# Kernel optimization log

Hardware: AMD Instinct MI355X
Metric: run time of the kernel (lower is better)

Reference implementation:

```python
import jax, jax.numpy as jnp
import numpy as np

VOXEL_SIZE = 96
SHARPNESS = 100.0
EPS = 1e-8


def _grid_coords(V):
    # matches torch: x fastest, normalized by (V-1); shape [V*V, 2] as (x, y)
    y, x = jnp.meshgrid(jnp.arange(V, dtype=jnp.float32), jnp.arange(V, dtype=jnp.float32), indexing='ij')
    return jnp.stack([x.ravel(), y.ravel()], axis=1) / float(V - 1)


def setup_inputs() -> dict:
    key = jax.random.key(0)
    k1, k2, k3 = jax.random.split(key, 3)
    B, N, P = 4, 32, 32
    polygons = jax.random.uniform(k1, (B, N, P, 2), dtype=jnp.float32)
    attributes = jax.random.uniform(k2, (B, 8), dtype=jnp.float32)
    validity_scores = jax.random.uniform(k3, (B, N), dtype=jnp.float32)
    return {"polygons": polygons, "attributes": attributes, "validity_scores": validity_scores}


def _polygon_masks(polygons, coords):
    # polygons: [B,N,P,2], coords: [M,2] -> soft occupancy masks [B,N,M]
    v0 = polygons                              # [B,N,P,2]
    v1 = jnp.roll(polygons, -1, axis=2)        # next vertex (closed loop)
    e = v1 - v0                                # edges [B,N,P,2]
    pts = coords[None, None, None]             # [1,1,1,M,2]
    v = pts - v0[:, :, :, None, :]             # [B,N,P,M,2]
    e_sq = (e * e).sum(-1) + EPS               # [B,N,P]
    t = (v * e[:, :, :, None, :]).sum(-1) / e_sq[..., None]   # [B,N,P,M]
    t = jnp.clip(t, 0.0, 1.0)
    proj = v0[:, :, :, None, :] + t[..., None] * e[:, :, :, None, :]
    diff = pts - proj
    dists = jnp.sqrt((diff * diff).sum(-1))    # [B,N,P,M]
    min_dist = dists.min(axis=2)               # [B,N,M] min over edges
    # ray-casting point-in-polygon (horizontal ray toward +x)
    x_pts = coords[:, 0]                        # [M]
    y_pts = coords[:, 1]
    x0, y0 = v0[..., 0:1], v0[..., 1:2]        # [B,N,P,1]
    x1, y1 = v1[..., 0:1], v1[..., 1:2]
    y_crosses = ((y0 <= y_pts) & (y1 > y_pts)) | ((y1 <= y_pts) & (y0 > y_pts))
    inter_x = x0 + (x1 - x0) * ((y_pts - y0) / (y1 - y0 + EPS))
    crossings = (inter_x > x_pts) & y_crosses  # [B,N,P,M]
    inside = (crossings.sum(axis=2) % 2) == 1  # [B,N,M]
    sdf = jnp.where(inside, -min_dist, min_dist)
    return jax.nn.sigmoid(-sdf * SHARPNESS)    # [B,N,M]


def reference(polygons, attributes, validity_scores):
    B = polygons.shape[0]
    V = VOXEL_SIZE
    coords = _grid_coords(V)                                   # [V*V, 2]
    masks = _polygon_masks(polygons, coords)                   # [B,N,M]
    valid = validity_scores >= 0.5                             # [B,N]
    combined = jnp.max(jnp.where(valid[:, :, None], masks, 0.0), axis=1)  # [B,M]
    combined = combined.reshape(B, V, V)                       # [B,H,W]
    # height extrusion: int(round(clamp(attr,0,1)*D)), clamped to [1,D]; non-differentiable
    norm_h = jnp.clip(attributes[:, 0], 0.0, 1.0)
    hv = jnp.clip(jnp.round(norm_h * V), 1.0, float(V))        # [B]
    hv = jax.lax.stop_gradient(hv)
    depth_mask = (jnp.arange(V, dtype=jnp.float32)[None, :] < hv[:, None]).astype(combined.dtype)  # [B,D]
    voxels = combined[:, None, :, :] * depth_mask[:, :, None, None]  # [B,D,H,W]
    return voxels
```

## Files before the change

kernel.cpp:

```cpp
#include <hip/hip_runtime.h>

#define V 96
#define VV (V * V)
#define B_ 4
#define N_ 32
#define P_ 32
#define BLOCKS_PER_BN (VV / 256)

__global__ __launch_bounds__(256) void mask_kernel(
    const float* __restrict__ poly,
    const float* __restrict__ validity,
    float* __restrict__ combined)
{
    const int bn  = blockIdx.x / BLOCKS_PER_BN;
    const int pix = (blockIdx.x % BLOCKS_PER_BN) * 256 + threadIdx.x;

    if (validity[bn] < 0.5f) return;

    __shared__ float sx0[P_], sy0[P_], sex[P_], sey[P_], srq[P_], sry[P_];
    if (threadIdx.x < P_) {
        const int p  = threadIdx.x;
        const int pn = (p + 1) & (P_ - 1);
        const float* base = poly + (size_t)bn * (P_ * 2);
        float x0 = base[p * 2],  y0 = base[p * 2 + 1];
        float x1 = base[pn * 2], y1 = base[pn * 2 + 1];
        float ex = x1 - x0, ey = y1 - y0;
        sx0[p] = x0; sy0[p] = y0; sex[p] = ex; sey[p] = ey;
        srq[p] = __builtin_amdgcn_rcpf(ex * ex + ey * ey + 1e-8f);
        sry[p] = __builtin_amdgcn_rcpf(ey + 1e-8f);
    }
    __syncthreads();

    const int py_i = pix / V, px_i = pix - py_i * V;
    const float px = (float)px_i / 95.0f;
    const float py = (float)py_i / 95.0f;

    float mind2 = 1e30f;
    int   par   = 0;

    #pragma unroll
    for (int p = 0; p < P_; ++p) {
        const int pn = (p + 1) & (P_ - 1);
        float x0 = sx0[p], y0 = sy0[p];
        float y1 = sy0[pn];
        float ex = sex[p], ey = sey[p];

        float vx = px - x0, vy = py - y0;
        float t  = (vx * ex + vy * ey) * srq[p];
        t = fminf(fmaxf(t, 0.0f), 1.0f);
        float dx = vx - t * ex, dy = vy - t * ey;
        float d2 = dx * dx + dy * dy;
        mind2 = fminf(mind2, d2);

        bool c0 = (y0 <= py);
        bool c1 = (y1 <= py);
        float inter_x = x0 + ex * ((py - y0) * sry[p]);
        par ^= (int)((c0 != c1) & (inter_x > px));
    }

    float mind = sqrtf(mind2);
    float sdf  = par ? -mind : mind;
    float m = 1.0f / (1.0f + __expf(sdf * 100.0f));

    if (m >= 1e-5f) {
        const int b = bn >> 5;
        atomicMax((unsigned int*)(combined + (size_t)b * VV + pix),
                  __float_as_uint(m));
    }
}

__global__ __launch_bounds__(256) void expand_kernel(
    const float* __restrict__ combined,
    const float* __restrict__ attr,
    float4* __restrict__ out)
{
    const int gid = blockIdx.x * 256 + threadIdx.x;
    const int row = gid / (V / 4);
    const int x4  = gid - row * (V / 4);
    const int y   = row % V;
    const int t_  = row / V;
    const int d   = t_ % V;
    const int b   = t_ / V;

    float a  = attr[b * 8];
    float nh = fminf(fmaxf(a, 0.0f), 1.0f);
    float hv = fminf(fmaxf(rintf(nh * (float)V), 1.0f), (float)V);
    float keep = ((float)d < hv) ? 1.0f : 0.0f;

    float4 c = ((const float4*)combined)[(size_t)b * (VV / 4) + y * (V / 4) + x4];
    out[gid] = make_float4(c.x * keep, c.y * keep, c.z * keep, c.w * keep);
}

extern "C" void kernel_launch(void* const* d_in, const int* in_sizes, int n_in,
                              void* d_out, int out_size, void* d_ws, size_t ws_size,
                              hipStream_t stream) {
    const float* polygons = (const float*)d_in[0];
    const float* attrs    = (const float*)d_in[1];
    const float* validity = (const float*)d_in[2];
    float* out = (float*)d_out;
    float* combined = (float*)d_ws;

    hipMemsetAsync(combined, 0, (size_t)B_ * VV * sizeof(float), stream);

    mask_kernel<<<B_ * N_ * BLOCKS_PER_BN, 256, 0, stream>>>(polygons, validity, combined);
    expand_kernel<<<(B_ * V * V * (V / 4)) / 256, 256, 0, stream>>>(combined, attrs, (float4*)out);
}
```

Before: 73.28 us.

## Fuse mask, max-reduction and depth extrusion into a single per-tile kernel

Replaces the memset, the per-polygon atomicMax mask kernel and the separate expand kernel with one kernel. Each block handles 64 pixels of one batch and compacts the valid polygons into a list. Four wave groups split those polygons, reduce their maxima in shared memory, then write the depth-extruded output directly. This removes two launches, the atomics and the round trip through the intermediate buffer. In exchange each block recomputes edge data for all 1024 edges of its batch, and the block count drops to 576.

```diff
diff --git a/kernel.cpp b/kernel.cpp
--- a/kernel.cpp
+++ b/kernel.cpp
@@ -2,93 +2,129 @@
 
 #define V 96
 #define VV (V * V)
+#define V3 (V * V * V)
 #define B_ 4
 #define N_ 32
 #define P_ 32
-#define BLOCKS_PER_BN (VV / 256)
+#define NE (N_ * P_)
+#define TILE 64
+#define TPB 256
+#define SPLITS 4
+#define TILES_PER_B (VV / TILE)
 
-__global__ __launch_bounds__(256) void mask_kernel(
+__global__ __launch_bounds__(TPB) void fused_kernel(
     const float* __restrict__ poly,
+    const float* __restrict__ attr,
     const float* __restrict__ validity,
-    float* __restrict__ combined)
+    float4* __restrict__ out)
 {
-    const int bn  = blockIdx.x / BLOCKS_PER_BN;
-    const int pix = (blockIdx.x % BLOCKS_PER_BN) * 256 + threadIdx.x;
+    __shared__ float4 se0[NE];
+    __shared__ float4 se1[NE];
+    __shared__ float2 sraw[NE];
+    __shared__ float  spart[SPLITS][TILE];
+    __shared__ __align__(16) float sfinal[TILE];
+    __shared__ int svalidIdx[N_];
+    __shared__ int scnt;
 
-    if (validity[bn] < 0.5f) return;
+    const int b       = blockIdx.x / TILES_PER_B;
+    const int tileInB = blockIdx.x - b * TILES_PER_B;
+    const int pix0    = tileInB * TILE;
+    const int tid     = threadIdx.x;
+    const int s       = tid >> 6;
+    const int lane    = tid & 63;
 
-    __shared__ float sx0[P_], sy0[P_], sex[P_], sey[P_], srq[P_], sry[P_];
-    if (threadIdx.x < P_) {
-        const int p  = threadIdx.x;
-        const int pn = (p + 1) & (P_ - 1);
-        const float* base = poly + (size_t)bn * (P_ * 2);
-        float x0 = base[p * 2],  y0 = base[p * 2 + 1];
-        float x1 = base[pn * 2], y1 = base[pn * 2 + 1];
-        float ex = x1 - x0, ey = y1 - y0;
-        sx0[p] = x0; sy0[p] = y0; sex[p] = ex; sey[p] = ey;
-        srq[p] = __builtin_amdgcn_rcpf(ex * ex + ey * ey + 1e-8f);
-        sry[p] = __builtin_amdgcn_rcpf(ey + 1e-8f);
+    {
+        const float4* pg = (const float4*)(poly + (size_t)b * (N_ * P_ * 2));
+        float4 q0 = pg[2 * tid];
+        float4 q1 = pg[2 * tid + 1];
+        float4* sr4 = (float4*)sraw;
+        sr4[2 * tid]     = q0;
+        sr4[2 * tid + 1] = q1;
+    }
+    if (tid < 64) {
+        bool v = (tid < N_) && (validity[b * N_ + tid] >= 0.5f);
+        unsigned long long m = __ballot(v);
+        if (v) {
+            int pos = __popcll(m & ((1ull << tid) - 1));
+            svalidIdx[pos] = tid;
+        }
+        if (tid == 0) scnt = (int)__popcll(m);
     }
     __syncthreads();
 
-    const int py_i = pix / V, px_i = pix - py_i * V;
+    #pragma unroll
+    for (int i = 0; i < 4; ++i) {
+        int e  = 4 * tid + i;
+        int p  = e & (P_ - 1);
+        int nb = e & ~(P_ - 1);
+        int en = nb | ((p + 1) & (P_ - 1));
+        float2 v0 = sraw[e];
+        float2 v1 = sraw[en];
+        float ex = v1.x - v0.x, ey = v1.y - v0.y;
+        se0[e] = make_float4(v0.x, v0.y, ex, ey);
+        se1[e] = make_float4(__builtin_amdgcn_rcpf(ex * ex + ey * ey + 1e-8f),
+                             __builtin_amdgcn_rcpf(ey + 1e-8f),
+                             v1.y,
+                             0.0f);
+    }
+    __syncthreads();
+
+    const int pixel = pix0 + lane;
+    const int py_i  = pixel / V;
+    const int px_i  = pixel - py_i * V;
     const float px = (float)px_i / 95.0f;
     const float py = (float)py_i / 95.0f;
 
-    float mind2 = 1e30f;
-    int   par   = 0;
+    const int cnt = scnt;
+    float pmax = 0.0f;
 
-    #pragma unroll
-    for (int p = 0; p < P_; ++p) {
-        const int pn = (p + 1) & (P_ - 1);
-        float x0 = sx0[p], y0 = sy0[p];
-        float y1 = sy0[pn];
-        float ex = sex[p], ey = sey[p];
-
-        float vx = px - x0, vy = py - y0;
-        float t  = (vx * ex + vy * ey) * srq[p];
-        t = fminf(fmaxf(t, 0.0f), 1.0f);
-        float dx = vx - t * ex, dy = vy - t * ey;
-        float d2 = dx * dx + dy * dy;
-        mind2 = fminf(mind2, d2);
-
-        bool c0 = (y0 <= py);
-        bool c1 = (y1 <= py);
-        float inter_x = x0 + ex * ((py - y0) * sry[p]);
-        par ^= (int)((c0 != c1) & (inter_x > px));
+    for (int j = s; j < cnt; j += SPLITS) {
+        const int base = svalidIdx[j] << 5;
+        float mind2 = 1e30f;
+        int par = 0;
+        #pragma unroll
+        for (int p = 0; p < P_; ++p) {
+            float4 e0 = se0[base + p];
+            float4 e1 = se1[base + p];
+            float vx = px - e0.x, vy = py - e0.y;
+            float t  = (vx * e0.z + vy * e0.w) * e1.x;
+            t = fminf(fmaxf(t, 0.0f), 1.0f);
+            float dx = vx - t * e0.z, dy = vy - t * e0.w;
+            float d2 = dx * dx + dy * dy;
+            mind2 = fminf(mind2, d2);
+            bool c0 = (e0.y <= py);
+            bool c1 = (e1.z <= py);
+            float inter_x = e0.x + e0.z * ((py - e0.y) * e1.y);
+            par ^= (int)((c0 != c1) & (inter_x > px));
+        }
+        float mind = sqrtf(mind2);
+        float sdf  = par ? -mind : mind;
+        float m = 1.0f / (1.0f + __expf(sdf * 100.0f));
+        pmax = fmaxf(pmax, m);
     }
 
-    float mind = sqrtf(mind2);
-    float sdf  = par ? -mind : mind;
-    float m = 1.0f / (1.0f + __expf(sdf * 100.0f));
-
-    if (m >= 1e-5f) {
-        const int b = bn >> 5;
-        atomicMax((unsigned int*)(combined + (size_t)b * VV + pix),
-                  __float_as_uint(m));
-    }
-}
-
-__global__ __launch_bounds__(256) void expand_kernel(
-    const float* __restrict__ combined,
-    const float* __restrict__ attr,
-    float4* __restrict__ out)
-{
-    const int gid = blockIdx.x * 256 + threadIdx.x;
-    const int row = gid / (V / 4);
-    const int x4  = gid - row * (V / 4);
-    const int y   = row % V;
-    const int t_  = row / V;
-    const int d   = t_ % V;
-    const int b   = t_ / V;
+    spart[s][lane] = pmax;
+    __syncthreads();
+    float f = fmaxf(fmaxf(spart[0][lane], spart[1][lane]),
+                    fmaxf(spart[2][lane], spart[3][lane]));
+    if (s == 0) sfinal[lane] = f;
+    __syncthreads();
 
     float a  = attr[b * 8];
     float nh = fminf(fmaxf(a, 0.0f), 1.0f);
     float hv = fminf(fmaxf(rintf(nh * (float)V), 1.0f), (float)V);
-    float keep = ((float)d < hv) ? 1.0f : 0.0f;
+    int hvi = (int)hv;
 
-    float4 c = ((const float4*)combined)[(size_t)b * (VV / 4) + y * (V / 4) + x4];
-    out[gid] = make_float4(c.x * keep, c.y * keep, c.z * keep, c.w * keep);
+    const float4* sf4 = (const float4*)sfinal;
+    const float4 val = sf4[lane & 15];
+    size_t obase = (size_t)b * (V3 / 4) + (size_t)(pix0 >> 2) + (lane & 15);
+    #pragma unroll
+    for (int k = 0; k < 6; ++k) {
+        int d = s * 24 + k * 4 + (lane >> 4);
+        float keep = (d < hvi) ? 1.0f : 0.0f;
+        out[obase + (size_t)d * (VV / 4)] =
+            make_float4(val.x * keep, val.y * keep, val.z * keep, val.w * keep);
+    }
 }
 
 extern "C" void kernel_launch(void* const* d_in, const int* in_sizes, int n_in,
@@ -97,11 +133,7 @@
     const float* polygons = (const float*)d_in[0];
     const float* attrs    = (const float*)d_in[1];
     const float* validity = (const float*)d_in[2];
-    float* out = (float*)d_out;
-    float* combined = (float*)d_ws;
+    float4* out = (float4*)d_out;
 
-    hipMemsetAsync(combined, 0, (size_t)B_ * VV * sizeof(float), stream);
-
-    mask_kernel<<<B_ * N_ * BLOCKS_PER_BN, 256, 0, stream>>>(polygons, validity, combined);
-    expand_kernel<<<(B_ * V * V * (V / 4)) / 256, 256, 0, stream>>>(combined, attrs, (float4*)out);
+    fused_kernel<<<B_ * TILES_PER_B, TPB, 0, stream>>>(polygons, attrs, validity, out);
 }
```

New measurement: 76.17 us. 3.9% more time.
